# Kernel tuning notes

Hardware: AMD Instinct MI355X
Metric: run time of the kernel (lower is better)

Reference implementation:

```python
import jax, jax.numpy as jnp
import numpy as np

B, N, F = 4096, 64, 128   # batch, max_neighbor, input feature dim
H, D = 8, 64              # num_heads, weight_dims (per head)
HD = H * D


def setup_inputs() -> dict:
    key = jax.random.key(0)
    k1, k2, k3, k4 = jax.random.split(key, 4)
    x = jax.random.normal(k1, (B, N, F), dtype=jnp.float32)
    W_lin = jax.random.normal(k2, (F, HD), dtype=jnp.float32) * (1.0 / np.sqrt(F))
    W_att = jax.random.normal(k3, (2 * HD, H), dtype=jnp.float32) * (1.0 / np.sqrt(2 * HD))
    mask = jax.random.randint(k4, (B, N), 0, 2, dtype=jnp.int32)
    return {"x": x, "W_lin": W_lin, "W_att": W_att, "mask": mask}


def reference(x, W_lin, W_att, mask):
    # dropout is identity (rate 0.0 / inference)
    lin = x @ W_lin                               # [B, N, H*D]
    # src node is neighbor slot 0 of each batch row (the Python-loop gather+tile)
    src = lin[:, 0, :]                            # [B, H*D]
    # attention_layer on concat([src, lin]) == src@W_att[:HD] + lin@W_att[HD:]
    att = src @ W_att[:HD]                        # [B, H]
    att = att[:, None, :] + lin @ W_att[HD:]      # [B, N, H]
    att = jnp.where(att >= 0, att, 0.2 * att)     # LeakyReLU(alpha=0.2)
    aw = jnp.transpose(att, (0, 2, 1))            # [B, H, N]  (split heads + squeeze)
    aw = aw + (mask == 0).astype(jnp.float32)[:, None, :] * (-1e9)
    aw = jax.nn.softmax(aw, axis=2)[..., None]    # [B, H, N, 1]
    lp = jnp.transpose(lin.reshape(B, N, H, D), (0, 2, 1, 3))  # [B, H, N, D]
    weighted = lp * aw                            # [B, H, N, D]
    # fusion 'concat': unstack heads, concat along last -> [B, N, H*D], then ReLU
    out = jnp.transpose(weighted, (0, 2, 1, 3)).reshape(B, N, HD)
    return jax.nn.relu(out)
```

## Files before the change

kernel.cpp:

```cpp
#include <hip/hip_runtime.h>


typedef _Float16 half8  __attribute__((ext_vector_type(8)));
typedef _Float16 half4v __attribute__((ext_vector_type(4)));
typedef float    f32x4  __attribute__((ext_vector_type(4)));

static constexpr int NSEQ  = 64;
static constexpr int FIN   = 128;
static constexpr int HDIM  = 512;
static constexpr int NHEAD = 8;
static constexpr int XS_LD = 136;

static constexpr int SMEM_BYTES = 39168;

__global__ __launch_bounds__(256) void prep_kernel(const float* __restrict__ wlin,
                                                   const float* __restrict__ watt,
                                                   _Float16* __restrict__ wlinT,
                                                   _Float16* __restrict__ waA)
{
    int t = blockIdx.x * 256 + threadIdx.x;
    if (t < HDIM * FIN) {
        int c = t >> 7;
        int k = t & 127;
        wlinT[t] = (_Float16)wlin[k * HDIM + c];
    }
    if (t < 16 * HDIM) {
        int i     = t & 3;
        int lane  = (t >> 2) & 63;
        int slice = t >> 8;
        int c = (slice >> 2) * 64 + (slice & 3) * 16 + (lane >> 4) * 4 + i;
        int j = lane & 15;
        float v = (j < NHEAD) ? watt[(HDIM + c) * NHEAD + j]
                              : watt[c * NHEAD + (j - NHEAD)];
        waA[t] = (_Float16)v;
    }
}

__global__ __launch_bounds__(512, 4) void fused_kernel(const float* __restrict__ x,
                                                       const _Float16* __restrict__ wlinT,
                                                       const _Float16* __restrict__ waA,
                                                       const int* __restrict__ mask,
                                                       float* __restrict__ out)
{
    __shared__ char smem[SMEM_BYTES] __attribute__((aligned(16)));
    _Float16* xs     = (_Float16*)smem;
    float*    attbuf = (float*)smem;
    float*    att_s  = (float*)(smem + 34816);

    const int b    = blockIdx.x;
    const int t    = threadIdx.x;
    const int lane = t & 63;
    const int w    = t >> 6;
    const int l15  = lane & 15;
    const int quad = lane >> 4;

    const int mv = mask[b * NSEQ + lane];

    const f32x4* xb = (const f32x4*)(x + (size_t)b * (NSEQ * FIN));
    #pragma unroll
    for (int it = 0; it < 4; ++it) {
        int i = it * 512 + t;
        f32x4 v = __builtin_nontemporal_load(&xb[i]);
        int n = i >> 5;
        int k = (i & 31) << 2;
        half4v hv;
        hv[0] = (_Float16)v[0]; hv[1] = (_Float16)v[1];
        hv[2] = (_Float16)v[2]; hv[3] = (_Float16)v[3];
        *(half4v*)(xs + n * XS_LD + k) = hv;
    }
    __syncthreads();

    f32x4 acc[4][4];
    #pragma unroll
    for (int mt = 0; mt < 4; ++mt)
        #pragma unroll
        for (int nt = 0; nt < 4; ++nt)
            acc[mt][nt] = (f32x4){0.f, 0.f, 0.f, 0.f};

    const int colbase = w * 64;
    #pragma unroll
    for (int ks = 0; ks < 4; ++ks) {
        const int k0 = ks * 32 + quad * 8;
        half8 a[4];
        #pragma unroll
        for (int mt = 0; mt < 4; ++mt)
            a[mt] = *(const half8*)(wlinT + (colbase + mt * 16 + l15) * FIN + k0);
        #pragma unroll
        for (int nt = 0; nt < 4; ++nt) {
            half8 bfr = *(const half8*)(xs + (nt * 16 + l15) * XS_LD + k0);
            #pragma unroll
            for (int mt = 0; mt < 4; ++mt)
                acc[mt][nt] = __builtin_amdgcn_mfma_f32_16x16x32_f16(a[mt], bfr, acc[mt][nt], 0, 0, 0);
        }
    }
    __syncthreads();

    {
        f32x4 T[4];
        #pragma unroll
        for (int nt = 0; nt < 4; ++nt) T[nt] = (f32x4){0.f, 0.f, 0.f, 0.f};
        #pragma unroll
        for (int mt = 0; mt < 4; ++mt) {
            half4v aF = *(const half4v*)(waA + ((w * 4 + mt) * 64 + lane) * 4);
            #pragma unroll
            for (int nt = 0; nt < 4; ++nt) {
                half4v bF;
                #pragma unroll
                for (int i = 0; i < 4; ++i) bF[i] = (_Float16)acc[mt][nt][i];
                T[nt] = __builtin_amdgcn_mfma_f32_16x16x16f16(aF, bF, T[nt], 0, 0, 0);
            }
        }
        #pragma unroll
        for (int nt = 0; nt < 4; ++nt)
            *(f32x4*)(attbuf + (w * 64 + nt * 16 + l15) * 16 + quad * 4) = T[nt];
    }
    __syncthreads();

    {
        int n  = t >> 3;
        int j0 = (t & 7) * 2;
        float s0 = 0.f, s1 = 0.f;
        #pragma unroll
        for (int ww = 0; ww < 8; ++ww) {
            const float* p = attbuf + (ww * 64 + n) * 16 + j0;
            s0 += p[0]; s1 += p[1];
        }
        att_s[n * 17 + j0]     = s0;
        att_s[n * 17 + j0 + 1] = s1;
    }
    __syncthreads();

    float aw_reg;
    {
        const float pen = (mv == 0) ? -1e9f : 0.0f;
        float a = att_s[lane * 17 + w] + att_s[8 + w];
        a = (a >= 0.0f) ? a : 0.2f * a;
        a += pen;
        float mx = a;
        #pragma unroll
        for (int off = 32; off > 0; off >>= 1)
            mx = fmaxf(mx, __shfl_xor(mx, off, 64));
        float e = __expf(a - mx);
        float s = e;
        #pragma unroll
        for (int off = 32; off > 0; off >>= 1)
            s += __shfl_xor(s, off, 64);
        aw_reg = e / s;
    }

    {
        float* ft = (float*)smem + w * (16 * 68);
        float* outb = out + (size_t)b * (NSEQ * HDIM);
        #pragma unroll
        for (int nt = 0; nt < 4; ++nt) {
            float awv = __shfl(aw_reg, nt * 16 + l15, 64);
            #pragma unroll
            for (int mt = 0; mt < 4; ++mt) {
                f32x4 o;
                #pragma unroll
                for (int i = 0; i < 4; ++i)
                    o[i] = fmaxf(acc[mt][nt][i] * awv, 0.0f);
                *(f32x4*)(ft + l15 * 68 + mt * 16 + quad * 4) = o;
            }
            #pragma unroll
            for (int s = 0; s < 4; ++s) {
                int r = s * 4 + quad;
                f32x4 v = *(const f32x4*)(ft + r * 68 + l15 * 4);
                int n = nt * 16 + r;
                __builtin_nontemporal_store(v, (f32x4*)(outb + n * HDIM + w * 64 + l15 * 4));
            }
        }
    }
}

extern "C" void kernel_launch(void* const* d_in, const int* in_sizes, int n_in,
                              void* d_out, int out_size, void* d_ws, size_t ws_size,
                              hipStream_t stream)
{
    const float* x    = (const float*)d_in[0];
    const float* wlin = (const float*)d_in[1];
    const float* watt = (const float*)d_in[2];
    const int*   mask = (const int*)d_in[3];
    float* out = (float*)d_out;

    _Float16* wlinT = (_Float16*)d_ws;
    _Float16* waA   = wlinT + HDIM * FIN;

    const int B = in_sizes[0] / (NSEQ * FIN);

    prep_kernel<<<256, 256, 0, stream>>>(wlin, watt, wlinT, waA);
    fused_kernel<<<B, 512, 0, stream>>>(x, wlinT, waA, mask, out);
}
```

Baseline: 638.0 us.

## Process four batches per block with register-staged prefetch of next x tile

```diff
diff --git a/kernel.cpp b/kernel.cpp
--- a/kernel.cpp
+++ b/kernel.cpp
@@ -5,13 +5,16 @@
 typedef _Float16 half4v __attribute__((ext_vector_type(4)));
 typedef float    f32x4  __attribute__((ext_vector_type(4)));
 
-static constexpr int NSEQ  = 64;
-static constexpr int FIN   = 128;
-static constexpr int HDIM  = 512;
-static constexpr int NHEAD = 8;
-static constexpr int XS_LD = 136;
-
-static constexpr int SMEM_BYTES = 39168;
+static constexpr int NSEQ   = 64;
+static constexpr int FIN    = 128;
+static constexpr int HDIM   = 512;
+static constexpr int NHEAD  = 8;
+static constexpr int XS_LD  = 136;
+static constexpr int NBATCH = 4;
+
+static constexpr int R_OFF      = 17408;
+static constexpr int ATT_OFF    = 52224;
+static constexpr int SMEM_BYTES = 56576;
 
 __global__ __launch_bounds__(256) void prep_kernel(const float* __restrict__ wlin,
                                                    const float* __restrict__ watt,
@@ -44,132 +47,165 @@
 {
     __shared__ char smem[SMEM_BYTES] __attribute__((aligned(16)));
     _Float16* xs     = (_Float16*)smem;
-    float*    attbuf = (float*)smem;
-    float*    att_s  = (float*)(smem + 34816);
-
-    const int b    = blockIdx.x;
+    float*    attbuf = (float*)(smem + R_OFF);
+    float*    att_s  = (float*)(smem + ATT_OFF);
+
     const int t    = threadIdx.x;
     const int lane = t & 63;
     const int w    = t >> 6;
     const int l15  = lane & 15;
     const int quad = lane >> 4;
 
-    const int mv = mask[b * NSEQ + lane];
-
-    const f32x4* xb = (const f32x4*)(x + (size_t)b * (NSEQ * FIN));
-    #pragma unroll
-    for (int it = 0; it < 4; ++it) {
-        int i = it * 512 + t;
-        f32x4 v = __builtin_nontemporal_load(&xb[i]);
-        int n = i >> 5;
-        int k = (i & 31) << 2;
-        half4v hv;
-        hv[0] = (_Float16)v[0]; hv[1] = (_Float16)v[1];
-        hv[2] = (_Float16)v[2]; hv[3] = (_Float16)v[3];
-        *(half4v*)(xs + n * XS_LD + k) = hv;
-    }
+    const int b0 = blockIdx.x * NBATCH;
+
+    {
+        const f32x4* xb = (const f32x4*)(x + (size_t)b0 * (NSEQ * FIN));
+        #pragma unroll
+        for (int j = 0; j < 4; ++j) {
+            int i = j * 512 + t;
+            f32x4 v = __builtin_nontemporal_load(&xb[i]);
+            int n = i >> 5;
+            int k = (i & 31) << 2;
+            half4v hv;
+            hv[0] = (_Float16)v[0]; hv[1] = (_Float16)v[1];
+            hv[2] = (_Float16)v[2]; hv[3] = (_Float16)v[3];
+            *(half4v*)(xs + n * XS_LD + k) = hv;
+        }
+    }
+    int mv = mask[b0 * NSEQ + lane];
     __syncthreads();
 
-    f32x4 acc[4][4];
-    #pragma unroll
-    for (int mt = 0; mt < 4; ++mt)
-        #pragma unroll
-        for (int nt = 0; nt < 4; ++nt)
-            acc[mt][nt] = (f32x4){0.f, 0.f, 0.f, 0.f};
-
-    const int colbase = w * 64;
-    #pragma unroll
-    for (int ks = 0; ks < 4; ++ks) {
-        const int k0 = ks * 32 + quad * 8;
-        half8 a[4];
+    #pragma unroll 1
+    for (int it = 0; it < NBATCH; ++it) {
+        const int b    = b0 + it;
+        const bool more = (it + 1 < NBATCH);
+
+        f32x4 acc[4][4];
         #pragma unroll
         for (int mt = 0; mt < 4; ++mt)
-            a[mt] = *(const half8*)(wlinT + (colbase + mt * 16 + l15) * FIN + k0);
+            #pragma unroll
+            for (int nt = 0; nt < 4; ++nt)
+                acc[mt][nt] = (f32x4){0.f, 0.f, 0.f, 0.f};
+
+        const int colbase = w * 64;
         #pragma unroll
-        for (int nt = 0; nt < 4; ++nt) {
-            half8 bfr = *(const half8*)(xs + (nt * 16 + l15) * XS_LD + k0);
+        for (int ks = 0; ks < 4; ++ks) {
+            const int k0 = ks * 32 + quad * 8;
+            half8 a[4];
             #pragma unroll
             for (int mt = 0; mt < 4; ++mt)
-                acc[mt][nt] = __builtin_amdgcn_mfma_f32_16x16x32_f16(a[mt], bfr, acc[mt][nt], 0, 0, 0);
-        }
-    }
-    __syncthreads();
-
-    {
-        f32x4 T[4];
-        #pragma unroll
-        for (int nt = 0; nt < 4; ++nt) T[nt] = (f32x4){0.f, 0.f, 0.f, 0.f};
-        #pragma unroll
-        for (int mt = 0; mt < 4; ++mt) {
-            half4v aF = *(const half4v*)(waA + ((w * 4 + mt) * 64 + lane) * 4);
+                a[mt] = *(const half8*)(wlinT + (colbase + mt * 16 + l15) * FIN + k0);
             #pragma unroll
             for (int nt = 0; nt < 4; ++nt) {
-                half4v bF;
-                #pragma unroll
-                for (int i = 0; i < 4; ++i) bF[i] = (_Float16)acc[mt][nt][i];
-                T[nt] = __builtin_amdgcn_mfma_f32_16x16x16f16(aF, bF, T[nt], 0, 0, 0);
-            }
-        }
-        #pragma unroll
-        for (int nt = 0; nt < 4; ++nt)
-            *(f32x4*)(attbuf + (w * 64 + nt * 16 + l15) * 16 + quad * 4) = T[nt];
-    }
-    __syncthreads();
-
-    {
-        int n  = t >> 3;
-        int j0 = (t & 7) * 2;
-        float s0 = 0.f, s1 = 0.f;
-        #pragma unroll
-        for (int ww = 0; ww < 8; ++ww) {
-            const float* p = attbuf + (ww * 64 + n) * 16 + j0;
-            s0 += p[0]; s1 += p[1];
-        }
-        att_s[n * 17 + j0]     = s0;
-        att_s[n * 17 + j0 + 1] = s1;
-    }
-    __syncthreads();
-
-    float aw_reg;
-    {
-        const float pen = (mv == 0) ? -1e9f : 0.0f;
-        float a = att_s[lane * 17 + w] + att_s[8 + w];
-        a = (a >= 0.0f) ? a : 0.2f * a;
-        a += pen;
-        float mx = a;
-        #pragma unroll
-        for (int off = 32; off > 0; off >>= 1)
-            mx = fmaxf(mx, __shfl_xor(mx, off, 64));
-        float e = __expf(a - mx);
-        float s = e;
-        #pragma unroll
-        for (int off = 32; off > 0; off >>= 1)
-            s += __shfl_xor(s, off, 64);
-        aw_reg = e / s;
-    }
-
-    {
-        float* ft = (float*)smem + w * (16 * 68);
-        float* outb = out + (size_t)b * (NSEQ * HDIM);
-        #pragma unroll
-        for (int nt = 0; nt < 4; ++nt) {
-            float awv = __shfl(aw_reg, nt * 16 + l15, 64);
+                half8 bfr = *(const half8*)(xs + (nt * 16 + l15) * XS_LD + k0);
+                #pragma unroll
+                for (int mt = 0; mt < 4; ++mt)
+                    acc[mt][nt] = __builtin_amdgcn_mfma_f32_16x16x32_f16(a[mt], bfr, acc[mt][nt], 0, 0, 0);
+            }
+        }
+
+        f32x4 stg[4];
+        int mv_next = 0;
+        if (more) {
+            const f32x4* xbn = (const f32x4*)(x + (size_t)(b + 1) * (NSEQ * FIN));
+            #pragma unroll
+            for (int j = 0; j < 4; ++j)
+                stg[j] = __builtin_nontemporal_load(&xbn[j * 512 + t]);
+            mv_next = mask[(b + 1) * NSEQ + lane];
+        }
+
+        {
+            f32x4 T[4];
+            #pragma unroll
+            for (int nt = 0; nt < 4; ++nt) T[nt] = (f32x4){0.f, 0.f, 0.f, 0.f};
             #pragma unroll
             for (int mt = 0; mt < 4; ++mt) {
-                f32x4 o;
-                #pragma unroll
-                for (int i = 0; i < 4; ++i)
-                    o[i] = fmaxf(acc[mt][nt][i] * awv, 0.0f);
-                *(f32x4*)(ft + l15 * 68 + mt * 16 + quad * 4) = o;
-            }
-            #pragma unroll
-            for (int s = 0; s < 4; ++s) {
-                int r = s * 4 + quad;
-                f32x4 v = *(const f32x4*)(ft + r * 68 + l15 * 4);
-                int n = nt * 16 + r;
-                __builtin_nontemporal_store(v, (f32x4*)(outb + n * HDIM + w * 64 + l15 * 4));
-            }
-        }
+                half4v aF = *(const half4v*)(waA + ((w * 4 + mt) * 64 + lane) * 4);
+                #pragma unroll
+                for (int nt = 0; nt < 4; ++nt) {
+                    half4v bF;
+                    #pragma unroll
+                    for (int i = 0; i < 4; ++i) bF[i] = (_Float16)acc[mt][nt][i];
+                    T[nt] = __builtin_amdgcn_mfma_f32_16x16x16f16(aF, bF, T[nt], 0, 0, 0);
+                }
+            }
+            #pragma unroll
+            for (int nt = 0; nt < 4; ++nt)
+                *(f32x4*)(attbuf + (w * 64 + nt * 16 + l15) * 16 + quad * 4) = T[nt];
+        }
+        __syncthreads();
+
+        {
+            int n  = t >> 3;
+            int j0 = (t & 7) * 2;
+            float s0 = 0.f, s1 = 0.f;
+            #pragma unroll
+            for (int ww = 0; ww < 8; ++ww) {
+                const float* p = attbuf + (ww * 64 + n) * 16 + j0;
+                s0 += p[0]; s1 += p[1];
+            }
+            att_s[n * 17 + j0]     = s0;
+            att_s[n * 17 + j0 + 1] = s1;
+        }
+        __syncthreads();
+
+        float aw_reg;
+        {
+            const float pen = (mv == 0) ? -1e9f : 0.0f;
+            float a = att_s[lane * 17 + w] + att_s[8 + w];
+            a = (a >= 0.0f) ? a : 0.2f * a;
+            a += pen;
+            float mx = a;
+            #pragma unroll
+            for (int off = 32; off > 0; off >>= 1)
+                mx = fmaxf(mx, __shfl_xor(mx, off, 64));
+            float e = __expf(a - mx);
+            float s = e;
+            #pragma unroll
+            for (int off = 32; off > 0; off >>= 1)
+                s += __shfl_xor(s, off, 64);
+            aw_reg = e / s;
+        }
+
+        if (more) {
+            #pragma unroll
+            for (int j = 0; j < 4; ++j) {
+                int i = j * 512 + t;
+                int n = i >> 5;
+                int k = (i & 31) << 2;
+                half4v hv;
+                hv[0] = (_Float16)stg[j][0]; hv[1] = (_Float16)stg[j][1];
+                hv[2] = (_Float16)stg[j][2]; hv[3] = (_Float16)stg[j][3];
+                *(half4v*)(xs + n * XS_LD + k) = hv;
+            }
+        }
+
+        {
+            float* ft = (float*)(smem + R_OFF) + w * (16 * 68);
+            float* outb = out + (size_t)b * (NSEQ * HDIM);
+            #pragma unroll
+            for (int nt = 0; nt < 4; ++nt) {
+                float awv = __shfl(aw_reg, nt * 16 + l15, 64);
+                #pragma unroll
+                for (int mt = 0; mt < 4; ++mt) {
+                    f32x4 o;
+                    #pragma unroll
+                    for (int i = 0; i < 4; ++i)
+                        o[i] = fmaxf(acc[mt][nt][i] * awv, 0.0f);
+                    *(f32x4*)(ft + l15 * 68 + mt * 16 + quad * 4) = o;
+                }
+                #pragma unroll
+                for (int s = 0; s < 4; ++s) {
+                    int r = s * 4 + quad;
+                    f32x4 v = *(const f32x4*)(ft + r * 68 + l15 * 4);
+                    int n = nt * 16 + r;
+                    __builtin_nontemporal_store(v, (f32x4*)(outb + n * HDIM + w * 64 + l15 * 4));
+                }
+            }
+        }
+
+        mv = mv_next;
+        __syncthreads();
     }
 }
 
@@ -189,5 +225,5 @@
     const int B = in_sizes[0] / (NSEQ * FIN);
 
     prep_kernel<<<256, 256, 0, stream>>>(wlin, watt, wlinT, waA);
-    fused_kernel<<<B, 512, 0, stream>>>(x, wlinT, waA, mask, out);
+    fused_kernel<<<B / NBATCH, 512, 0, stream>>>(x, wlinT, waA, mask, out);
 }
```

Result: slower. 725.6 us (+13.7%).
